# Performance work log

Hardware: AMD Instinct MI355X
Metric: run time of the kernel (lower is better)

The kernel has to match this reference:

```python
import jax, jax.numpy as jnp
import numpy as np

DIM = 64
WS = 8    # window_size
SS = 4    # shift_size


def _conv(x, w, pad, groups=1):
    return jax.lax.conv_general_dilated(
        x, w, (1, 1), ((pad, pad), (pad, pad)),
        dimension_numbers=('NCHW', 'OIHW', 'NCHW'),
        feature_group_count=groups)


def _window_partition(x, ws):
    # x: (B, C, H, W) -> (B*Hn*Wn, C, ws, ws), with bottom/right padding
    B, C, H, W = x.shape
    pb = (-H) % ws
    pr = (-W) % ws
    x = jnp.pad(x, ((0, 0), (0, 0), (0, pb), (0, pr)))
    Hp, Wp = H + pb, W + pr
    x = x.reshape(B, C, Hp // ws, ws, Wp // ws, ws).transpose(0, 1, 2, 4, 3, 5)
    return x.reshape(-1, C, ws, ws)


def _window_reverse(wins, ws, H, W):
    pb = (-H) % ws
    pr = (-W) % ws
    Hp, Wp = H + pb, W + pr
    B = wins.shape[0] // ((Hp // ws) * (Wp // ws))
    x = wins.reshape(B, -1, Hp // ws, Wp // ws, ws, ws).transpose(0, 1, 2, 4, 3, 5)
    x = x.reshape(B, -1, Hp, Wp)
    return x[:, :, :H, :W]


def _create_mask(H, W, ws, ss):
    # Swin-style additive mask, computed statically with numpy
    Hp = int(np.ceil(H / ws)) * ws
    Wp = int(np.ceil(W / ws)) * ws
    m = np.zeros((Hp, Wp), dtype=np.float32)
    slices = (slice(0, -ws), slice(-ws, -ss), slice(-ss, None))
    cnt = 0
    for hs in slices:
        for wsl in slices:
            m[hs, wsl] = cnt
            cnt += 1
    mw = m.reshape(Hp // ws, ws, Wp // ws, ws).transpose(0, 2, 1, 3).reshape(-1, ws * ws)
    diff = mw[:, None, :] - mw[:, :, None]
    return jnp.asarray(np.where(diff != 0, -100.0, 0.0).astype(np.float32))


def _l2norm(x):
    # matches torch F.normalize(dim=-1, eps=1e-12)
    return x / jnp.maximum(jnp.linalg.norm(x, axis=-1, keepdims=True), 1e-12)


def _win_attn(xw, w_qkv, w_dw, w_proj, ws, mask, b):
    # xw: (N, C, ws, ws) windows
    C = xw.shape[1]
    qkv = _conv(_conv(xw, w_qkv, 0), w_dw, 1, groups=3 * C)
    q, k, v = jnp.split(qkv, 3, axis=1)
    N = q.shape[0]
    hw = ws * ws
    q = _l2norm(q.reshape(N, C, hw))
    k = _l2norm(k.reshape(N, C, hw))
    v = v.reshape(N, C, hw)
    attn = jnp.einsum('nci,ncj->nij', q, k) / ws  # (N, hw, hw)
    if mask is not None:
        attn = (attn.reshape(b, -1, hw, hw) + mask[None]).reshape(-1, hw, hw)
    attn = jax.nn.softmax(attn, axis=-1)
    out = jnp.einsum('nci,nij->ncj', v, attn).reshape(N, C, ws, ws)
    return _conv(out, w_proj, 1)


def _forward(x, w_qkv0, w_dw0, w_proj0, w_qkv1, w_dw1, w_proj1):
    b, c, h, w = x.shape
    # pass 1: unshifted windows
    xw = _window_partition(x, WS)
    out = _win_attn(xw, w_qkv0, w_dw0, w_proj0, WS, None, b)
    out = _window_reverse(out, WS, h, w)
    # pass 2: shifted windows with Swin mask
    shift = jnp.roll(out, (-SS, -SS), axis=(2, 3))
    sw = _window_partition(shift, WS)
    mask = _create_mask(h, w, WS, SS)
    out = _win_attn(sw, w_qkv1, w_dw1, w_proj1, WS, mask, b)
    out = _window_reverse(out, WS, h, w)
    return jnp.roll(out, (SS, SS), axis=(2, 3))


def setup_inputs() -> dict:
    key = jax.random.key(0)
    ks = jax.random.split(key, 7)
    C = DIM
    s = 0.05
    return {
        'x': jax.random.normal(ks[0], (8, C, 256, 256), jnp.float32),
        'w_qkv0': jax.random.normal(ks[1], (3 * C, C, 1, 1), jnp.float32) * s,
        'w_dw0': jax.random.normal(ks[2], (3 * C, 1, 3, 3), jnp.float32) * s,
        'w_proj0': jax.random.normal(ks[3], (C, C, 3, 3), jnp.float32) * s,
        'w_qkv1': jax.random.normal(ks[4], (3 * C, C, 1, 1), jnp.float32) * s,
        'w_dw1': jax.random.normal(ks[5], (3 * C, 1, 3, 3), jnp.float32) * s,
        'w_proj1': jax.random.normal(ks[6], (C, C, 3, 3), jnp.float32) * s,
    }


def reference(x, w_qkv0, w_dw0, w_proj0, w_qkv1, w_dw1, w_proj1):
    return _forward(x, w_qkv0, w_dw0, w_proj0, w_qkv1, w_dw1, w_proj1)
```

## Files before the change

kernel.cpp:

```cpp
#include <hip/hip_runtime.h>


typedef __attribute__((ext_vector_type(8))) short bf8;
typedef __attribute__((ext_vector_type(4))) float f32x4;
#define MFMA(a, b, c) __builtin_amdgcn_mfma_f32_16x16x32_bf16(a, b, c, 0, 0, 0)

__device__ __forceinline__ int xkey(int p) { return ((p >> 3) ^ p) & 7; }
__device__ __forceinline__ int xswz(int p, int c) { return p * 64 + (c ^ (xkey(p) << 3)); }
__device__ __forceinline__ int kswz(int r, int c) {
    return r * 32 + (c ^ ((((r >> 3) ^ (r >> 1)) & 3) << 3));
}
__device__ __forceinline__ int sswz(int ch, int p) {
    return ch * 64 + (p ^ (((ch >> 1) & 7) << 2));
}
__device__ __forceinline__ int jswz(int ch, int p) {
    return ch * 64 + (p ^ (((ch >> 1) & 7) << 3));
}

__device__ __forceinline__ unsigned cvtpk(float a, float b) {
    unsigned r;
    asm("v_cvt_pk_bf16_f32 %0, %1, %2" : "=v"(r) : "v"(a), "v"(b));
    return r;
}

__device__ __forceinline__ void bsplit(float f, short& h, short& l) {
    unsigned u = __float_as_uint(f);
    unsigned hb = (u + 0x7FFFu + ((u >> 16) & 1u)) >> 16;
    float hf = __uint_as_float(hb << 16);
    float r = f - hf;
    unsigned u2 = __float_as_uint(r);
    unsigned lb = (u2 + 0x7FFFu + ((u2 >> 16) & 1u)) >> 16;
    h = (short)hb; l = (short)lb;
}
__device__ __forceinline__ void bsplit2(float a, float b, unsigned& hw, unsigned& lw) {
    hw = cvtpk(a, b);
    float ra = a - __uint_as_float(hw << 16);
    float rb = b - __uint_as_float(hw & 0xFFFF0000u);
    lw = cvtpk(ra, rb);
}

__global__ void k_fq(const float* __restrict__ wq, short* __restrict__ oh, short* __restrict__ ol) {
    int bx = blockIdx.x;
    int kk = bx / 12, tt = bx % 12;
    int tid = threadIdx.x;
    int lane = tid >> 3, j = tid & 7;
    int oc = tt * 16 + (lane & 15);
    int ic = kk * 32 + ((lane >> 4) << 3) + j;
    short h, l; bsplit(wq[oc * 64 + ic], h, l);
    oh[bx * 512 + tid] = h; ol[bx * 512 + tid] = l;
}
__global__ void k_fp(const float* __restrict__ wp, short* __restrict__ oh, short* __restrict__ ol) {
    int bx = blockIdx.x;
    int tap = bx >> 3, kk = (bx >> 2) & 1, tt = bx & 3;
    int tid = threadIdx.x;
    int lane = tid >> 3, j = tid & 7;
    int oc = tt * 16 + (lane & 15);
    int ic = kk * 32 + ((lane >> 4) << 3) + j;
    short h, l; bsplit(wp[(oc * 64 + ic) * 9 + tap], h, l);
    oh[bx * 512 + tid] = h; ol[bx * 512 + tid] = l;
}

__device__ __forceinline__ void dw_one(const float* scr, const float* wd,
                                       int ch, int row, float o[8]) {
    float w9[9];
    #pragma unroll
    for (int tp = 0; tp < 9; ++tp) w9[tp] = wd[tp];
    float e[3][10];
    #pragma unroll
    for (int k3 = 0; k3 < 3; ++k3) {
        int rr = row - 1 + k3;
        e[k3][0] = 0.f; e[k3][9] = 0.f;
        if ((unsigned)rr < 8u) {
            float4 a = *(const float4*)&scr[sswz(ch, rr * 8)];
            float4 b = *(const float4*)&scr[sswz(ch, rr * 8 + 4)];
            e[k3][1] = a.x; e[k3][2] = a.y; e[k3][3] = a.z; e[k3][4] = a.w;
            e[k3][5] = b.x; e[k3][6] = b.y; e[k3][7] = b.z; e[k3][8] = b.w;
        } else {
            #pragma unroll
            for (int q2 = 1; q2 < 9; ++q2) e[k3][q2] = 0.f;
        }
    }
    #pragma unroll
    for (int s = 0; s < 8; ++s) {
        float a = 0.f;
        #pragma unroll
        for (int k3 = 0; k3 < 3; ++k3)
            #pragma unroll
            for (int dx = 0; dx < 3; ++dx)
                a = fmaf(w9[k3 * 3 + dx], e[k3][s + dx], a);
        o[s] = a;
    }
}

__device__ __forceinline__ float norm8(const float d[8]) {
    float ss = 0.f;
    #pragma unroll
    for (int s = 0; s < 8; ++s) ss = fmaf(d[s], d[s], ss);
    ss += __shfl_xor(ss, 1); ss += __shfl_xor(ss, 2); ss += __shfl_xor(ss, 4);
    return fmaxf(sqrtf(ss), 1e-12f);
}

__device__ __forceinline__ void p2_chunk32(const short* XTh, const short* XTl,
                                           const short* bqh, const short* bql,
                                           float* scr, int chunk,
                                           int mh, int nh, int col, int quad, int qo8, int lane)
{
    f32x4 acc[2];
    #pragma unroll
    for (int mt = 0; mt < 2; ++mt) acc[mt] = (f32x4){0.f, 0.f, 0.f, 0.f};
    int ad0[2];
    #pragma unroll
    for (int mt = 0; mt < 2; ++mt) {
        int row = (mh * 2 + mt) * 16 + col;
        ad0[mt] = row * 64 + (qo8 ^ (xkey(row) << 3));
    }
    #pragma unroll
    for (int kk = 0; kk < 2; ++kk) {
        bf8 Ah[2], Al[2];
        #pragma unroll
        for (int mt = 0; mt < 2; ++mt) {
            int ad = ad0[mt] ^ (kk << 5);
            Ah[mt] = *(const bf8*)&XTh[ad];
            Al[mt] = *(const bf8*)&XTl[ad];
        }
        int tt = chunk * 2 + nh;
        bf8 Bh = *(const bf8*)&bqh[((kk * 12 + tt) * 64 + lane) * 8];
        bf8 Bl = *(const bf8*)&bql[((kk * 12 + tt) * 64 + lane) * 8];
        #pragma unroll
        for (int mt = 0; mt < 2; ++mt) {
            acc[mt] = MFMA(Ah[mt], Bh, acc[mt]);
            acc[mt] = MFMA(Ah[mt], Bl, acc[mt]);
            acc[mt] = MFMA(Al[mt], Bh, acc[mt]);
        }
    }
    #pragma unroll
    for (int mt = 0; mt < 2; ++mt) {
        int ocl = nh * 16 + col;
        int p0 = (mh * 2 + mt) * 16 + quad * 4;
        *(f32x4*)&scr[sswz(ocl, p0)] = acc[mt];
    }
}

template<int SHIFT, int MASK, int ROLL>
__global__ __launch_bounds__(256, 4)
void k_fused(const float* __restrict__ in,
             const short* __restrict__ bqh, const short* __restrict__ bql,
             const float* __restrict__ wdw,
             const short* __restrict__ bph, const short* __restrict__ bpl,
             float* __restrict__ out)
{
    __shared__ __align__(16) char smem[32768];
    short* XTh = (short*)smem;
    short* XTl = (short*)(smem + 8192);
    float* bufA = (float*)(smem + 16384);
    float* bufB = (float*)(smem + 24576);
    short* K0h = (short*)(smem + 16384);
    short* K0l = (short*)(smem + 20480);
    short* K1h = (short*)(smem + 24576);
    short* K1l = (short*)(smem + 28672);
    short* vbh = (short*)(smem + 16384);
    short* vbl = (short*)(smem + 20480);
    short* PTf = (short*)(smem + 24576);
    short* PTg = (short*)(smem + 28672);
    float* projo = (float*)(smem + 16384);

    const int tid = threadIdx.x, lane = tid & 63, wv = tid >> 6;
    const int col = lane & 15, quad = lane >> 4, qo8 = quad * 8;
    const int mh = wv & 1, nh = wv >> 1;
    const int ch = tid >> 3, rrow = tid & 7;
    const int n = blockIdx.x;
    const int b = n >> 10, c = (n >> 4) & 63, t = n & 15;
    const size_t base = ((size_t)(b * 64 + c)) << 16;

    #pragma unroll
    for (int k = 0; k < 16; k += 2) {
        int o0 = tid + k * 256, o1 = o0 + 256;
        float v0, v1;
        if (SHIFT == 0) {
            const float* src = in + base + (size_t)t * 4096;
            v0 = src[o0]; v1 = src[o1];
        } else {
            int hi0 = o0 >> 11, r0 = (o0 >> 8) & 7, lo0 = (o0 >> 3) & 31, s0 = o0 & 7;
            int hi1 = o1 >> 11, r1 = (o1 >> 8) & 7, lo1 = (o1 >> 3) & 31, s1 = o1 & 7;
            v0 = in[base + (size_t)(((t * 16 + hi0 * 8 + r0) + SHIFT) & 255) * 256
                         + (((lo0 * 8 + s0) + SHIFT) & 255)];
            v1 = in[base + (size_t)(((t * 16 + hi1 * 8 + r1) + SHIFT) & 255) * 256
                         + (((lo1 * 8 + s1) + SHIFT) & 255)];
        }
        unsigned hw, lw; bsplit2(v0, v1, hw, lw);
        int hi0 = o0 >> 11, r0 = (o0 >> 8) & 7, lo0 = (o0 >> 3) & 31, s0 = o0 & 7;
        int hi1 = o1 >> 11, r1 = (o1 >> 8) & 7, lo1 = (o1 >> 3) & 31, s1 = o1 & 7;
        int ad0 = xswz(r0 * 8 + s0, hi0 * 32 + lo0);
        int ad1 = xswz(r1 * 8 + s1, hi1 * 32 + lo1);
        XTh[ad0] = (short)hw; XTh[ad1] = (short)(hw >> 16);
        XTl[ad0] = (short)lw; XTl[ad1] = (short)(lw >> 16);
    }
    __syncthreads();

    unsigned qAh[4], qAl[4], qBh[4], qBl[4];
    unsigned vAh[4], vAl[4], vBh[4], vBl[4];
    unsigned k0h[4], k0l[4], k1h[4], k1l[4];
    float nqA, nqB;

    p2_chunk32(XTh, XTl, bqh, bql, bufA, 0, mh, nh, col, quad, qo8, lane);
    __syncthreads();
    p2_chunk32(XTh, XTl, bqh, bql, bufB, 1, mh, nh, col, quad, qo8, lane);
    {
        float d[8];
        dw_one(bufA, wdw + ch * 9, ch, rrow, d);
        nqA = norm8(d);
        #pragma unroll
        for (int q2 = 0; q2 < 4; ++q2) bsplit2(d[2 * q2], d[2 * q2 + 1], qAh[q2], qAl[q2]);
    }
    __syncthreads();
    p2_chunk32(XTh, XTl, bqh, bql, bufA, 4, mh, nh, col, quad, qo8, lane);
    {
        float d[8];
        dw_one(bufB, wdw + (32 + ch) * 9, ch, rrow, d);
        nqB = norm8(d);
        #pragma unroll
        for (int q2 = 0; q2 < 4; ++q2) bsplit2(d[2 * q2], d[2 * q2 + 1], qBh[q2], qBl[q2]);
    }
    __syncthreads();
    p2_chunk32(XTh, XTl, bqh, bql, bufB, 5, mh, nh, col, quad, qo8, lane);
    {
        float d[8];
        dw_one(bufA, wdw + (128 + ch) * 9, ch, rrow, d);
        #pragma unroll
        for (int q2 = 0; q2 < 4; ++q2) bsplit2(d[2 * q2], d[2 * q2 + 1], vAh[q2], vAl[q2]);
    }
    __syncthreads();
    p2_chunk32(XTh, XTl, bqh, bql, bufA, 2, mh, nh, col, quad, qo8, lane);
    {
        float d[8];
        dw_one(bufB, wdw + (160 + ch) * 9, ch, rrow, d);
        #pragma unroll
        for (int q2 = 0; q2 < 4; ++q2) bsplit2(d[2 * q2], d[2 * q2 + 1], vBh[q2], vBl[q2]);
    }
    __syncthreads();
    p2_chunk32(XTh, XTl, bqh, bql, bufB, 3, mh, nh, col, quad, qo8, lane);
    {
        float d[8];
        dw_one(bufA, wdw + (64 + ch) * 9, ch, rrow, d);
        float sc = 0.125f / (nqA * norm8(d));
        #pragma unroll
        for (int s = 0; s < 8; ++s) d[s] *= sc;
        #pragma unroll
        for (int q2 = 0; q2 < 4; ++q2) bsplit2(d[2 * q2], d[2 * q2 + 1], k0h[q2], k0l[q2]);
    }
    __syncthreads();
    {
        float d[8];
        dw_one(bufB, wdw + (96 + ch) * 9, ch, rrow, d);
        float sc = 0.125f / (nqB * norm8(d));
        #pragma unroll
        for (int s = 0; s < 8; ++s) d[s] *= sc;
        #pragma unroll
        for (int q2 = 0; q2 < 4; ++q2) bsplit2(d[2 * q2], d[2 * q2 + 1], k1h[q2], k1l[q2]);
    }
    #pragma unroll
    for (int q2 = 0; q2 < 4; ++q2) {
        int p0 = rrow * 8 + 2 * q2;
        int a0 = kswz(p0, ch), a1 = kswz(p0 + 1, ch);
        K0h[a0] = (short)k0h[q2]; K0h[a1] = (short)(k0h[q2] >> 16);
        K0l[a0] = (short)k0l[q2]; K0l[a1] = (short)(k0l[q2] >> 16);
        int x0 = xswz(p0, ch), x1 = xswz(p0 + 1, ch);
        XTh[x0] = (short)qAh[q2]; XTh[x1] = (short)(qAh[q2] >> 16);
        XTl[x0] = (short)qAl[q2]; XTl[x1] = (short)(qAl[q2] >> 16);
        int cg = 32 + ch;
        int y0 = xswz(p0, cg), y1 = xswz(p0 + 1, cg);
        XTh[y0] = (short)qBh[q2]; XTh[y1] = (short)(qBh[q2] >> 16);
        XTl[y0] = (short)qBl[q2]; XTl[y1] = (short)(qBl[q2] >> 16);
    }
    __syncthreads();
    #pragma unroll
    for (int q2 = 0; q2 < 4; ++q2) {
        int p0 = rrow * 8 + 2 * q2;
        int a0 = kswz(p0, ch), a1 = kswz(p0 + 1, ch);
        K1h[a0] = (short)k1h[q2]; K1h[a1] = (short)(k1h[q2] >> 16);
        K1l[a0] = (short)k1l[q2]; K1l[a1] = (short)(k1l[q2] >> 16);
    }
    __syncthreads();

    f32x4 at[4];
    #pragma unroll
    for (int nt = 0; nt < 4; ++nt) at[nt] = (f32x4){0.f, 0.f, 0.f, 0.f};
    {
        bf8 Ah[2], Al[2];
        int rowA = wv * 16 + col;
        int adA0 = rowA * 64 + (qo8 ^ (xkey(rowA) << 3));
        #pragma unroll
        for (int kk = 0; kk < 2; ++kk) {
            int ad = adA0 ^ (kk << 5);
            Ah[kk] = *(const bf8*)&XTh[ad];
            Al[kk] = *(const bf8*)&XTl[ad];
        }
        #pragma unroll
        for (int kk = 0; kk < 2; ++kk) {
            const short* Bph = kk ? K1h : K0h;
            const short* Bpl = kk ? K1l : K0l;
            #pragma unroll
            for (int nt = 0; nt < 4; ++nt) {
                int rowB = nt * 16 + col;
                int ad = kswz(rowB, qo8);
                bf8 Bh = *(const bf8*)&Bph[ad];
                bf8 Bl = *(const bf8*)&Bpl[ad];
                at[nt] = MFMA(Ah[kk], Bh, at[nt]);
                at[nt] = MFMA(Ah[kk], Bl, at[nt]);
                at[nt] = MFMA(Al[kk], Bh, at[nt]);
            }
        }
    }
    if (MASK) {
        const int widx = n & 1023;
        const int hn_m = widx >> 5, wn_m = widx & 31;
        #pragma unroll
        for (int nt = 0; nt < 4; ++nt) {
            int j = nt * 16 + col;
            int rj = ((hn_m == 31) ? (((j >> 3) < 4) ? 1 : 2) : 0) * 3
                   + ((wn_m == 31) ? (((j & 7) < 4) ? 1 : 2) : 0);
            #pragma unroll
            for (int rg = 0; rg < 4; ++rg) {
                int i = wv * 16 + quad * 4 + rg;
                int ri = ((hn_m == 31) ? (((i >> 3) < 4) ? 1 : 2) : 0) * 3
                       + ((wn_m == 31) ? (((i & 7) < 4) ? 1 : 2) : 0);
                if (ri != rj) at[nt][rg] = at[nt][rg] - 100.f;
            }
        }
    }
    unsigned Ph[4][2], Pl[4][2];
    {
        float Pv[4][4];
        #pragma unroll
        for (int rg = 0; rg < 4; ++rg) {
            float m = fmaxf(fmaxf(at[0][rg], at[1][rg]), fmaxf(at[2][rg], at[3][rg]));
            m = fmaxf(m, __shfl_xor(m, 1)); m = fmaxf(m, __shfl_xor(m, 2));
            m = fmaxf(m, __shfl_xor(m, 4)); m = fmaxf(m, __shfl_xor(m, 8));
            float e0 = __expf(at[0][rg] - m), e1 = __expf(at[1][rg] - m);
            float e2 = __expf(at[2][rg] - m), e3 = __expf(at[3][rg] - m);
            float s = e0 + e1 + e2 + e3;
            s += __shfl_xor(s, 1); s += __shfl_xor(s, 2);
            s += __shfl_xor(s, 4); s += __shfl_xor(s, 8);
            float is = 1.0f / s;
            Pv[0][rg] = e0 * is; Pv[1][rg] = e1 * is; Pv[2][rg] = e2 * is; Pv[3][rg] = e3 * is;
        }
        #pragma unroll
        for (int nt = 0; nt < 4; ++nt)
            #pragma unroll
            for (int rp = 0; rp < 2; ++rp)
                bsplit2(Pv[nt][2 * rp], Pv[nt][2 * rp + 1], Ph[nt][rp], Pl[nt][rp]);
    }
    __syncthreads();

    f32x4 av[2][2];
    #pragma unroll
    for (int mt = 0; mt < 2; ++mt)
        #pragma unroll
        for (int nt = 0; nt < 2; ++nt) av[mt][nt] = (f32x4){0.f, 0.f, 0.f, 0.f};
    #pragma unroll
    for (int ih = 0; ih < 2; ++ih) {
        if ((rrow >> 2) == ih) {
            int rl = rrow & 3;
            int adA = kswz(ch, rl * 8);
            *(uint4*)&vbh[adA] = (uint4){vAh[0], vAh[1], vAh[2], vAh[3]};
            *(uint4*)&vbl[adA] = (uint4){vAl[0], vAl[1], vAl[2], vAl[3]};
            int adB = kswz(32 + ch, rl * 8);
            *(uint4*)&vbh[adB] = (uint4){vBh[0], vBh[1], vBh[2], vBh[3]};
            *(uint4*)&vbl[adB] = (uint4){vBl[0], vBl[1], vBl[2], vBl[3]};
        }
        if ((wv >> 1) == ih) {
            #pragma unroll
            for (int nt = 0; nt < 4; ++nt) {
                int j = nt * 16 + col;
                #pragma unroll
                for (int rp = 0; rp < 2; ++rp) {
                    int il = (wv & 1) * 16 + quad * 4 + 2 * rp;
                    int ad = kswz(j, il);
                    *(unsigned*)&PTf[ad] = Ph[nt][rp];
                    *(unsigned*)&PTg[ad] = Pl[nt][rp];
                }
            }
        }
        __syncthreads();
        {
            bf8 Ah[2], Al[2], Bh[2], Bl[2];
            #pragma unroll
            for (int mt = 0; mt < 2; ++mt) {
                int row = (mh * 2 + mt) * 16 + col;
                int ad = kswz(row, qo8);
                Ah[mt] = *(const bf8*)&vbh[ad];
                Al[mt] = *(const bf8*)&vbl[ad];
            }
            #pragma unroll
            for (int nt = 0; nt < 2; ++nt) {
                int rowB = (nh * 2 + nt) * 16 + col;
                int ad = kswz(rowB, qo8);
                Bh[nt] = *(const bf8*)&PTf[ad];
                Bl[nt] = *(const bf8*)&PTg[ad];
            }
            #pragma unroll
            for (int mt = 0; mt < 2; ++mt)
                #pragma unroll
                for (int nt = 0; nt < 2; ++nt) {
                    av[mt][nt] = MFMA(Ah[mt], Bh[nt], av[mt][nt]);
                    av[mt][nt] = MFMA(Ah[mt], Bl[nt], av[mt][nt]);
                    av[mt][nt] = MFMA(Al[mt], Bh[nt], av[mt][nt]);
                }
        }
        __syncthreads();
    }
    #pragma unroll
    for (int nt = 0; nt < 2; ++nt) {
        int j = (nh * 2 + nt) * 16 + col;
        #pragma unroll
        for (int mt = 0; mt < 2; ++mt) {
            int c0 = (mh * 2 + mt) * 16 + quad * 4;
            #pragma unroll
            for (int rp = 0; rp < 2; ++rp) {
                unsigned hw, lw; bsplit2(av[mt][nt][2 * rp], av[mt][nt][2 * rp + 1], hw, lw);
                int ad = j * 64 + ((c0 + 2 * rp) ^ (xkey(j) << 3));
                *(unsigned*)&XTh[ad] = hw;
                *(unsigned*)&XTl[ad] = lw;
            }
        }
    }
    if (tid < 32) ((unsigned*)(smem + 16384))[tid] = 0u;
    __syncthreads();

    {
        f32x4 ap[2][2];
        #pragma unroll
        for (int mt = 0; mt < 2; ++mt)
            #pragma unroll
            for (int nt = 0; nt < 2; ++nt) ap[mt][nt] = (f32x4){0.f, 0.f, 0.f, 0.f};
        const int smc = col & 7;
        #pragma unroll 1
        for (int tap = 0; tap < 9; ++tap) {
            int dy = (tap >= 6) ? 1 : ((tap >= 3) ? 0 : -1);
            int dx = tap - (dy + 1) * 3 - 1;
            int bh0[2], bl0[2];
            #pragma unroll
            for (int mt = 0; mt < 2; ++mt) {
                int rr = (mh * 2 + mt) * 2 + (col >> 3) + dy;
                int ss = smc + dx;
                bool ok = ((unsigned)rr < 8u) && ((unsigned)ss < 8u);
                int row = rr * 8 + ss;
                int ra_h = ok ? row : 128;
                int ra_l = ok ? row : 64;
                bh0[mt] = ra_h * 64 + (qo8 ^ (xkey(ra_h) << 3));
                bl0[mt] = ra_l * 64 + (qo8 ^ (xkey(ra_l) << 3));
            }
            #pragma unroll
            for (int kk = 0; kk < 2; ++kk) {
                bf8 Bh[2], Bl[2], Ah[2], Al[2];
                #pragma unroll
                for (int nt = 0; nt < 2; ++nt) {
                    int bi = (((tap * 2 + kk) * 4 + (nh * 2 + nt)) * 64 + lane) * 8;
                    Bh[nt] = *(const bf8*)&bph[bi];
                    Bl[nt] = *(const bf8*)&bpl[bi];
                }
                #pragma unroll
                for (int mt = 0; mt < 2; ++mt) {
                    Ah[mt] = *(const bf8*)&XTh[bh0[mt] ^ (kk << 5)];
                    Al[mt] = *(const bf8*)&XTl[bl0[mt] ^ (kk << 5)];
                }
                #pragma unroll
                for (int mt = 0; mt < 2; ++mt)
                    #pragma unroll
                    for (int nt = 0; nt < 2; ++nt) {
                        ap[mt][nt] = MFMA(Ah[mt], Bh[nt], ap[mt][nt]);
                        ap[mt][nt] = MFMA(Ah[mt], Bl[nt], ap[mt][nt]);
                        ap[mt][nt] = MFMA(Al[mt], Bh[nt], ap[mt][nt]);
                    }
            }
        }
        __syncthreads();
        #pragma unroll
        for (int nt = 0; nt < 2; ++nt) {
            int oc = (nh * 2 + nt) * 16 + col;
            #pragma unroll
            for (int mt = 0; mt < 2; ++mt) {
                int p0 = (mh * 2 + mt) * 16 + quad * 4;
                *(f32x4*)&projo[jswz(oc, p0)] = ap[mt][nt];
            }
        }
    }
    __syncthreads();

    #pragma unroll
    for (int k = 0; k < 16; ++k) {
        int o = tid + k * 256;
        int hi = o >> 11, r = (o >> 8) & 7, lo = (o >> 3) & 31, s = o & 7;
        int c2 = hi * 32 + lo;
        float v = projo[jswz(c2, r * 8 + s)];
        if (ROLL == 0) {
            float* dst = out + base + (size_t)t * 4096;
            dst[o] = v;
        } else {
            int h2 = t * 16 + hi * 8 + r, w2 = lo * 8 + s;
            out[base + (size_t)((h2 + ROLL) & 255) * 256 + ((w2 + ROLL) & 255)] = v;
        }
    }
}

extern "C" void kernel_launch(void* const* d_in, const int* in_sizes, int n_in,
                              void* d_out, int out_size, void* d_ws, size_t ws_size,
                              hipStream_t stream)
{
    const float* x      = (const float*)d_in[0];
    const float* wqkv0  = (const float*)d_in[1];
    const float* wdw0   = (const float*)d_in[2];
    const float* wproj0 = (const float*)d_in[3];
    const float* wqkv1  = (const float*)d_in[4];
    const float* wdw1   = (const float*)d_in[5];
    const float* wproj1 = (const float*)d_in[6];
    float* out = (float*)d_out;

    float* tmp = (float*)d_ws;
    short* fb  = (short*)(tmp + 33554432);
    short* bq0h = fb;
    short* bq0l = fb + 12288;
    short* bq1h = fb + 24576;
    short* bq1l = fb + 36864;
    short* bp0h = fb + 49152;
    short* bp0l = fb + 86016;
    short* bp1h = fb + 122880;
    short* bp1l = fb + 159744;

    hipLaunchKernelGGL(k_fq, dim3(24), dim3(512), 0, stream, wqkv0, bq0h, bq0l);
    hipLaunchKernelGGL(k_fq, dim3(24), dim3(512), 0, stream, wqkv1, bq1h, bq1l);
    hipLaunchKernelGGL(k_fp, dim3(72), dim3(512), 0, stream, wproj0, bp0h, bp0l);
    hipLaunchKernelGGL(k_fp, dim3(72), dim3(512), 0, stream, wproj1, bp1h, bp1l);

    hipLaunchKernelGGL(HIP_KERNEL_NAME(k_fused<0, 0, 0>), dim3(8192), dim3(256), 0, stream,
                       x, bq0h, bq0l, wdw0, bp0h, bp0l, tmp);
    hipLaunchKernelGGL(HIP_KERNEL_NAME(k_fused<4, 1, 4>), dim3(8192), dim3(256), 0, stream,
                       tmp, bq1h, bq1l, wdw1, bp1h, bp1l, out);
}
```

Measured before the change: 610.0 us.

## Stage V and P fully in LDS for single-pass PV and add MFMA priority hints

Shared memory is re-laid out so V goes into the freed X buffer and the full 64x64 P transpose goes into the upper half. The PV product then runs as one pass over K instead of two half-passes with a barrier between them. The PV output moves to a separate region, and the zero-padding addresses in the projection conv are changed to match. s_setprio hints are added around the MFMA loops so waves issuing matrix ops get scheduling priority. This removes one barrier and some branching per block, but changes the LDS aliasing, which risks hazards if any region is still live.

```diff
diff --git a/kernel.cpp b/kernel.cpp
--- a/kernel.cpp
+++ b/kernel.cpp
@@ -114,6 +114,7 @@
         int row = (mh * 2 + mt) * 16 + col;
         ad0[mt] = row * 64 + (qo8 ^ (xkey(row) << 3));
     }
+    __builtin_amdgcn_s_setprio(1);
     #pragma unroll
     for (int kk = 0; kk < 2; ++kk) {
         bf8 Ah[2], Al[2];
@@ -133,6 +134,7 @@
             acc[mt] = MFMA(Al[mt], Bh, acc[mt]);
         }
     }
+    __builtin_amdgcn_s_setprio(0);
     #pragma unroll
     for (int mt = 0; mt < 2; ++mt) {
         int ocl = nh * 16 + col;
@@ -158,10 +160,12 @@
     short* K0l = (short*)(smem + 20480);
     short* K1h = (short*)(smem + 24576);
     short* K1l = (short*)(smem + 28672);
-    short* vbh = (short*)(smem + 16384);
-    short* vbl = (short*)(smem + 20480);
-    short* PTf = (short*)(smem + 24576);
-    short* PTg = (short*)(smem + 28672);
+    short* vbh = (short*)smem;
+    short* vbl = (short*)(smem + 8192);
+    short* PTh = (short*)(smem + 16384);
+    short* PTl = (short*)(smem + 24576);
+    short* YTh = (short*)(smem + 16384);
+    short* YTl = (short*)(smem + 24576);
     float* projo = (float*)(smem + 16384);
 
     const int tid = threadIdx.x, lane = tid & 63, wv = tid >> 6;
@@ -295,6 +299,7 @@
             Ah[kk] = *(const bf8*)&XTh[ad];
             Al[kk] = *(const bf8*)&XTl[ad];
         }
+        __builtin_amdgcn_s_setprio(1);
         #pragma unroll
         for (int kk = 0; kk < 2; ++kk) {
             const short* Bph = kk ? K1h : K0h;
@@ -310,6 +315,7 @@
                 at[nt] = MFMA(Al[kk], Bh, at[nt]);
             }
         }
+        __builtin_amdgcn_s_setprio(0);
     }
     if (MASK) {
         const int widx = n & 1023;
@@ -352,51 +358,58 @@
     }
     __syncthreads();
 
+    {
+        int adA = ch * 64 + ((rrow * 8) ^ (xkey(ch) << 3));
+        *(uint4*)&vbh[adA] = (uint4){vAh[0], vAh[1], vAh[2], vAh[3]};
+        *(uint4*)&vbl[adA] = (uint4){vAl[0], vAl[1], vAl[2], vAl[3]};
+        int cg = 32 + ch;
+        int adB = cg * 64 + ((rrow * 8) ^ (xkey(cg) << 3));
+        *(uint4*)&vbh[adB] = (uint4){vBh[0], vBh[1], vBh[2], vBh[3]};
+        *(uint4*)&vbl[adB] = (uint4){vBl[0], vBl[1], vBl[2], vBl[3]};
+    }
+    #pragma unroll
+    for (int nt = 0; nt < 4; ++nt) {
+        int j = nt * 16 + col;
+        #pragma unroll
+        for (int rp = 0; rp < 2; ++rp) {
+            int i0 = wv * 16 + quad * 4 + 2 * rp;
+            int ad = j * 64 + (i0 ^ (xkey(j) << 3));
+            *(unsigned*)&PTh[ad] = Ph[nt][rp];
+            *(unsigned*)&PTl[ad] = Pl[nt][rp];
+        }
+    }
+    __syncthreads();
+
     f32x4 av[2][2];
     #pragma unroll
     for (int mt = 0; mt < 2; ++mt)
         #pragma unroll
         for (int nt = 0; nt < 2; ++nt) av[mt][nt] = (f32x4){0.f, 0.f, 0.f, 0.f};
-    #pragma unroll
-    for (int ih = 0; ih < 2; ++ih) {
-        if ((rrow >> 2) == ih) {
-            int rl = rrow & 3;
-            int adA = kswz(ch, rl * 8);
-            *(uint4*)&vbh[adA] = (uint4){vAh[0], vAh[1], vAh[2], vAh[3]};
-            *(uint4*)&vbl[adA] = (uint4){vAl[0], vAl[1], vAl[2], vAl[3]};
-            int adB = kswz(32 + ch, rl * 8);
-            *(uint4*)&vbh[adB] = (uint4){vBh[0], vBh[1], vBh[2], vBh[3]};
-            *(uint4*)&vbl[adB] = (uint4){vBl[0], vBl[1], vBl[2], vBl[3]};
-        }
-        if ((wv >> 1) == ih) {
-            #pragma unroll
-            for (int nt = 0; nt < 4; ++nt) {
-                int j = nt * 16 + col;
-                #pragma unroll
-                for (int rp = 0; rp < 2; ++rp) {
-                    int il = (wv & 1) * 16 + quad * 4 + 2 * rp;
-                    int ad = kswz(j, il);
-                    *(unsigned*)&PTf[ad] = Ph[nt][rp];
-                    *(unsigned*)&PTg[ad] = Pl[nt][rp];
-                }
-            }
-        }
-        __syncthreads();
-        {
+    {
+        int adA0[2], adB0[2];
+        #pragma unroll
+        for (int mt = 0; mt < 2; ++mt) {
+            int row = (mh * 2 + mt) * 16 + col;
+            adA0[mt] = row * 64 + (qo8 ^ (xkey(row) << 3));
+        }
+        #pragma unroll
+        for (int nt = 0; nt < 2; ++nt) {
+            int rowB = (nh * 2 + nt) * 16 + col;
+            adB0[nt] = rowB * 64 + (qo8 ^ (xkey(rowB) << 3));
+        }
+        __builtin_amdgcn_s_setprio(1);
+        #pragma unroll
+        for (int kk = 0; kk < 2; ++kk) {
             bf8 Ah[2], Al[2], Bh[2], Bl[2];
             #pragma unroll
             for (int mt = 0; mt < 2; ++mt) {
-                int row = (mh * 2 + mt) * 16 + col;
-                int ad = kswz(row, qo8);
-                Ah[mt] = *(const bf8*)&vbh[ad];
-                Al[mt] = *(const bf8*)&vbl[ad];
+                Ah[mt] = *(const bf8*)&vbh[adA0[mt] ^ (kk << 5)];
+                Al[mt] = *(const bf8*)&vbl[adA0[mt] ^ (kk << 5)];
             }
             #pragma unroll
             for (int nt = 0; nt < 2; ++nt) {
-                int rowB = (nh * 2 + nt) * 16 + col;
-                int ad = kswz(rowB, qo8);
-                Bh[nt] = *(const bf8*)&PTf[ad];
-                Bl[nt] = *(const bf8*)&PTg[ad];
+                Bh[nt] = *(const bf8*)&PTh[adB0[nt] ^ (kk << 5)];
+                Bl[nt] = *(const bf8*)&PTl[adB0[nt] ^ (kk << 5)];
             }
             #pragma unroll
             for (int mt = 0; mt < 2; ++mt)
@@ -407,8 +420,10 @@
                     av[mt][nt] = MFMA(Al[mt], Bh[nt], av[mt][nt]);
                 }
         }
-        __syncthreads();
-    }
+        __builtin_amdgcn_s_setprio(0);
+    }
+    __syncthreads();
+
     #pragma unroll
     for (int nt = 0; nt < 2; ++nt) {
         int j = (nh * 2 + nt) * 16 + col;
@@ -419,12 +434,12 @@
             for (int rp = 0; rp < 2; ++rp) {
                 unsigned hw, lw; bsplit2(av[mt][nt][2 * rp], av[mt][nt][2 * rp + 1], hw, lw);
                 int ad = j * 64 + ((c0 + 2 * rp) ^ (xkey(j) << 3));
-                *(unsigned*)&XTh[ad] = hw;
-                *(unsigned*)&XTl[ad] = lw;
-            }
-        }
-    }
-    if (tid < 32) ((unsigned*)(smem + 16384))[tid] = 0u;
+                *(unsigned*)&YTh[ad] = hw;
+                *(unsigned*)&YTl[ad] = lw;
+            }
+        }
+    }
+    if (tid < 32) ((unsigned*)smem)[tid] = 0u;
     __syncthreads();
 
     {
@@ -445,10 +460,9 @@
                 int ss = smc + dx;
                 bool ok = ((unsigned)rr < 8u) && ((unsigned)ss < 8u);
                 int row = rr * 8 + ss;
-                int ra_h = ok ? row : 128;
-                int ra_l = ok ? row : 64;
-                bh0[mt] = ra_h * 64 + (qo8 ^ (xkey(ra_h) << 3));
-                bl0[mt] = ra_l * 64 + (qo8 ^ (xkey(ra_l) << 3));
+                int good = row * 64 + (qo8 ^ (xkey(row) << 3));
+                bh0[mt] = ok ? good : (qo8 - 8192);
+                bl0[mt] = ok ? good : (qo8 - 12288);
             }
             #pragma unroll
             for (int kk = 0; kk < 2; ++kk) {
@@ -461,9 +475,10 @@
                 }
                 #pragma unroll
                 for (int mt = 0; mt < 2; ++mt) {
-                    Ah[mt] = *(const bf8*)&XTh[bh0[mt] ^ (kk << 5)];
-                    Al[mt] = *(const bf8*)&XTl[bl0[mt] ^ (kk << 5)];
+                    Ah[mt] = *(const bf8*)&YTh[bh0[mt] ^ (kk << 5)];
+                    Al[mt] = *(const bf8*)&YTl[bl0[mt] ^ (kk << 5)];
                 }
+                __builtin_amdgcn_s_setprio(1);
                 #pragma unroll
                 for (int mt = 0; mt < 2; ++mt)
                     #pragma unroll
@@ -472,6 +487,7 @@
                         ap[mt][nt] = MFMA(Ah[mt], Bl[nt], ap[mt][nt]);
                         ap[mt][nt] = MFMA(Al[mt], Bh[nt], ap[mt][nt]);
                     }
+                __builtin_amdgcn_s_setprio(0);
             }
         }
         __syncthreads();
```

Result: slower. 629.2 us (+3.2%).
